# Kernel optimization log

Hardware: AMD Instinct MI355X
Metric: run time of the kernel (lower is better)

Reference implementation:

```python
import jax, jax.numpy as jnp
import numpy as np

B = 2
C = 256
NH = 8
DH = C // NH
NL = 4
NP = 4
NLAYERS = 6
DFF = 1024
SHAPES = [(128, 128), (64, 64), (32, 32), (16, 16)]
LQ = sum(h * w for h, w in SHAPES)
STARTS = np.cumsum([0] + [h * w for h, w in SHAPES])[:-1].tolist()


def _ln(x, g, b, eps=1e-5):
    mu = jnp.mean(x, -1, keepdims=True)
    var = jnp.mean((x - mu) ** 2, -1, keepdims=True)
    return (x - mu) * jax.lax.rsqrt(var + eps) * g + b


def _ref_points():
    # centers of each cell, normalized to [0,1]; valid_ratios == 1 (masks=None path)
    pts = []
    for (h, w) in SHAPES:
        ry = (np.arange(h) + 0.5) / h
        rx = (np.arange(w) + 0.5) / w
        gy, gx = np.meshgrid(ry, rx, indexing='ij')
        pts.append(np.stack([gx.reshape(-1), gy.reshape(-1)], -1))
    return jnp.asarray(np.concatenate(pts, 0), jnp.float32)  # [LQ,2] (x,y)


def _bilinear(vf, loc, Hl, Wl):
    # vf: [B,NH,S,DH] flattened level features; loc: [B,LQ,NH,NP,2] in [0,1]
    # grid_sample semantics: bilinear, zero padding, align_corners=False
    x = loc[..., 0] * Wl - 0.5
    y = loc[..., 1] * Hl - 0.5
    x0 = jnp.floor(x)
    y0 = jnp.floor(y)
    wx = x - x0
    wy = y - y0
    out = 0.0
    for dx, dy, w in ((0, 0, (1 - wx) * (1 - wy)), (1, 0, wx * (1 - wy)),
                      (0, 1, (1 - wx) * wy), (1, 1, wx * wy)):
        xi = x0 + dx
        yi = y0 + dy
        valid = (xi >= 0) & (xi < Wl) & (yi >= 0) & (yi < Hl)
        idx = (jnp.clip(yi, 0, Hl - 1) * Wl + jnp.clip(xi, 0, Wl - 1)).astype(jnp.int32)
        idx = jnp.transpose(idx, (0, 2, 1, 3)).reshape(B, NH, -1)  # [B,NH,LQ*NP]
        g = jnp.take_along_axis(vf, idx[..., None], axis=2)        # [B,NH,LQ*NP,DH]
        wgt = jnp.transpose(w * valid, (0, 2, 1, 3)).reshape(B, NH, -1)
        out = out + g * wgt[..., None]
    return out.reshape(B, NH, LQ, NP, DH)


def _forward(src0, src1, src2, src3, pos0, pos1, pos2, pos3, level_embed,
             Woff, boff, Wattn, battn, Wval, bval, Wout, bout,
             g1, b1, Wff1, bff1, Wff2, bff2, g2, b2):
    srcs = [src0, src1, src2, src3]
    poss = [pos0, pos1, pos2, pos3]
    src = jnp.concatenate([s.reshape(B, C, -1).transpose(0, 2, 1) for s in srcs], 1)
    pos = jnp.concatenate([p.reshape(B, C, -1).transpose(0, 2, 1) + level_embed[l][None, None]
                           for l, p in enumerate(poss)], 1)
    ref = _ref_points()  # [LQ,2]
    norm_wh = jnp.asarray([[w, h] for (h, w) in SHAPES], jnp.float32)  # offset_normalizer
    x = src
    for l in range(NLAYERS):
        q = x + pos
        off = (q @ Woff[l] + boff[l]).reshape(B, LQ, NH, NL, NP, 2)
        attn = jax.nn.softmax((q @ Wattn[l] + battn[l]).reshape(B, LQ, NH, NL * NP), -1)
        attn = attn.reshape(B, LQ, NH, NL, NP)
        val = (x @ Wval[l] + bval[l]).reshape(B, LQ, NH, DH)
        loc = ref[None, :, None, None, None, :] + off / norm_wh[None, None, None, :, None, :]
        out = jnp.zeros((B, NH, LQ, DH), x.dtype)
        for lv, (h, w) in enumerate(SHAPES):
            s0 = STARTS[lv]
            vf = val[:, s0:s0 + h * w].transpose(0, 2, 1, 3)   # [B,NH,S,DH]
            samp = _bilinear(vf, loc[:, :, :, lv], h, w)       # [B,NH,LQ,NP,DH]
            a = attn[:, :, :, lv].transpose(0, 2, 1, 3)        # [B,NH,LQ,NP]
            out = out + jnp.einsum('bhqpd,bhqp->bhqd', samp, a)
        out = out.transpose(0, 2, 1, 3).reshape(B, LQ, C) @ Wout[l] + bout[l]
        x = _ln(x + out, g1[l], b1[l])
        ff = jax.nn.relu(x @ Wff1[l] + bff1[l]) @ Wff2[l] + bff2[l]
        x = _ln(x + ff, g2[l], b2[l])
    return x


def setup_inputs() -> dict:
    key = jax.random.key(0)
    ks = jax.random.split(key, 20)
    d = {}
    for i, (h, w) in enumerate(SHAPES):
        d[f'src{i}'] = jax.random.normal(ks[i], (B, C, h, w), jnp.float32)
        d[f'pos{i}'] = jax.random.normal(ks[4 + i], (B, C, h, w), jnp.float32) * 0.1
    d['level_embed'] = jax.random.normal(ks[8], (NL, C), jnp.float32)

    def lin(k, fi, fo, scale=None):
        s = scale if scale is not None else 1.0 / np.sqrt(fi)
        return jax.random.normal(k, (NLAYERS, fi, fo), jnp.float32) * s

    d['Woff'] = lin(ks[9], C, NH * NL * NP * 2, 0.01)
    d['boff'] = jax.random.uniform(ks[10], (NLAYERS, NH * NL * NP * 2), jnp.float32, -0.5, 0.5)
    d['Wattn'] = lin(ks[11], C, NH * NL * NP)
    d['battn'] = jnp.zeros((NLAYERS, NH * NL * NP), jnp.float32)
    d['Wval'] = lin(ks[12], C, C)
    d['bval'] = jnp.zeros((NLAYERS, C), jnp.float32)
    d['Wout'] = lin(ks[13], C, C)
    d['bout'] = jnp.zeros((NLAYERS, C), jnp.float32)
    d['g1'] = jnp.ones((NLAYERS, C), jnp.float32)
    d['b1'] = jnp.zeros((NLAYERS, C), jnp.float32)
    d['Wff1'] = lin(ks[14], C, DFF)
    d['bff1'] = jnp.zeros((NLAYERS, DFF), jnp.float32)
    d['Wff2'] = lin(ks[15], DFF, C)
    d['bff2'] = jnp.zeros((NLAYERS, C), jnp.float32)
    d['g2'] = jnp.ones((NLAYERS, C), jnp.float32)
    d['b2'] = jnp.zeros((NLAYERS, C), jnp.float32)
    return d


def reference(src0, src1, src2, src3, pos0, pos1, pos2, pos3, level_embed,
              Woff, boff, Wattn, battn, Wval, bval, Wout, bout,
              g1, b1, Wff1, bff1, Wff2, bff2, g2, b2):
    return _forward(src0, src1, src2, src3, pos0, pos1, pos2, pos3, level_embed,
                    Woff, boff, Wattn, battn, Wval, bval, Wout, bout,
                    g1, b1, Wff1, bff1, Wff2, bff2, g2, b2)
```

## Files before the change

kernel.cpp:

```cpp
#include <hip/hip_runtime.h>
#include <hip/hip_bf16.h>
#include <hip/hip_fp16.h>
#include <math.h>

namespace {
constexpr int B_   = 2;
constexpr int C_   = 256;
constexpr int NH_  = 8;
constexpr int DH_  = 32;
constexpr int NP_  = 4;
constexpr int DFF_ = 1024;
constexpr int LQ_  = 21760;
constexpr int M_   = B_ * LQ_;
}

typedef __bf16  bf16x8 __attribute__((ext_vector_type(8)));
typedef short   s16x8  __attribute__((ext_vector_type(8)));
typedef float   f32x4  __attribute__((ext_vector_type(4)));

static __device__ __forceinline__ unsigned short f2bf(float f) {
    return __builtin_bit_cast(unsigned short, __float2bfloat16(f));
}
static __device__ __forceinline__ float bf2f(unsigned short u) {
    return __bfloat162float(__builtin_bit_cast(__hip_bfloat16, u));
}

__global__ void k_wt(const float* __restrict__ in, __hip_bfloat16* __restrict__ out,
                     int K, int N, int outStride)
{
    __shared__ float tile[32][33];
    int n0 = blockIdx.x * 32, k0 = blockIdx.y * 32;
    const float* inl = in + (size_t)blockIdx.z * K * N;
    __hip_bfloat16* outl = out + (size_t)blockIdx.z * outStride;
    for (int i = threadIdx.y; i < 32; i += 8)
        tile[i][threadIdx.x] = inl[(size_t)(k0 + i) * N + n0 + threadIdx.x];
    __syncthreads();
    for (int i = threadIdx.y; i < 32; i += 8)
        outl[(size_t)(n0 + i) * K + k0 + threadIdx.x] = __float2bfloat16(tile[threadIdx.x][i]);
}

__global__ __launch_bounds__(256) void k_assemble2(
    const float* __restrict__ s0, const float* __restrict__ s1,
    const float* __restrict__ s2, const float* __restrict__ s3,
    const float* __restrict__ p0, const float* __restrict__ p1,
    const float* __restrict__ p2, const float* __restrict__ p3,
    const float* __restrict__ lev, float* __restrict__ x,
    __hip_bfloat16* __restrict__ xbf, __hip_bfloat16* __restrict__ posbf,
    __hip_bfloat16* __restrict__ qbf)
{
    int bid = blockIdx.x;
    int lv, rem, HW, S0;
    const float *sp, *pp;
    if (bid < 8192)       { lv = 0; rem = bid;         HW = 16384; S0 = 0;     sp = s0; pp = p0; }
    else if (bid < 10240) { lv = 1; rem = bid - 8192;  HW = 4096;  S0 = 16384; sp = s1; pp = p1; }
    else if (bid < 10752) { lv = 2; rem = bid - 10240; HW = 1024;  S0 = 20480; sp = s2; pp = p2; }
    else                  { lv = 3; rem = bid - 10752; HW = 256;   S0 = 21504; sp = s3; pp = p3; }
    int sptiles = HW >> 5;
    int spt = rem % sptiles;
    int ct  = (rem / sptiles) & 7;
    int b   = rem / (sptiles * 8);
    int sp0 = spt * 32, c0 = ct * 32;

    __shared__ float ts[32][33], tp[32][33];
    int tx = threadIdx.x & 31, ty = threadIdx.x >> 5;
#pragma unroll
    for (int i = 0; i < 4; i++) {
        int c = c0 + ty + i * 8;
        size_t si = ((size_t)(b * C_ + c)) * HW + sp0 + tx;
        ts[ty + i * 8][tx] = sp[si];
        tp[ty + i * 8][tx] = pp[si];
    }
    __syncthreads();
#pragma unroll
    for (int i = 0; i < 4; i++) {
        int s = S0 + sp0 + ty + i * 8;
        int c = c0 + tx;
        float sv = ts[tx][ty + i * 8];
        float pv = tp[tx][ty + i * 8] + lev[lv * C_ + c];
        size_t idx = ((size_t)(b * LQ_ + s)) * C_ + c;
        x[idx]     = sv;
        xbf[idx]   = __float2bfloat16(sv);
        posbf[idx] = __float2bfloat16(pv);
        qbf[idx]   = __float2bfloat16(sv + pv);
    }
}

template<bool RELU, bool BF16OUT>
__global__ __launch_bounds__(256) void k_gemm_mfma(
    const __hip_bfloat16* __restrict__ A,
    const __hip_bfloat16* __restrict__ Wt,
    const float* __restrict__ bias,
    void* __restrict__ Co,
    int M, int N, int K)
{
    __shared__ char As[128 * 128];
    __shared__ char Bs[128 * 128];
    int t = threadIdx.x, w = t >> 6, lane = t & 63;
    int m0 = blockIdx.x * 128, n0 = blockIdx.y * 128;
    int wm = w >> 1, wn = w & 1;

    f32x4 acc[4][4] = {};

    int rowoff  = lane >> 3;
    int colswz  = ((lane & 7) ^ (lane >> 3)) << 3;

    for (int kt = 0; kt < K; kt += 64) {
#pragma unroll
        for (int j = 0; j < 4; j++) {
            int rowbase = w * 32 + j * 8;
            const __hip_bfloat16* srcA = A  + (size_t)(m0 + rowbase + rowoff) * K + kt + colswz;
            const __hip_bfloat16* srcB = Wt + (size_t)(n0 + rowbase + rowoff) * K + kt + colswz;
            __builtin_amdgcn_global_load_lds(
                (const __attribute__((address_space(1))) void*)srcA,
                (__attribute__((address_space(3))) void*)(As + rowbase * 128), 16, 0, 0);
            __builtin_amdgcn_global_load_lds(
                (const __attribute__((address_space(1))) void*)srcB,
                (__attribute__((address_space(3))) void*)(Bs + rowbase * 128), 16, 0, 0);
        }
        __syncthreads();
#pragma unroll
        for (int k0 = 0; k0 < 64; k0 += 32) {
            int kb = k0 * 2 + (lane >> 4) * 16;
            bf16x8 af[4], bfr[4];
#pragma unroll
            for (int mi = 0; mi < 4; mi++) {
                int r = wm * 64 + mi * 16 + (lane & 15);
                s16x8 raw = *(const s16x8*)(As + r * 128 + (kb ^ ((r & 7) << 4)));
                af[mi] = __builtin_bit_cast(bf16x8, raw);
            }
#pragma unroll
            for (int ni = 0; ni < 4; ni++) {
                int r = wn * 64 + ni * 16 + (lane & 15);
                s16x8 raw = *(const s16x8*)(Bs + r * 128 + (kb ^ ((r & 7) << 4)));
                bfr[ni] = __builtin_bit_cast(bf16x8, raw);
            }
#pragma unroll
            for (int mi = 0; mi < 4; mi++)
#pragma unroll
                for (int ni = 0; ni < 4; ni++)
                    acc[mi][ni] = __builtin_amdgcn_mfma_f32_16x16x32_bf16(
                        af[mi], bfr[ni], acc[mi][ni], 0, 0, 0);
        }
        __syncthreads();
    }

#pragma unroll
    for (int ni = 0; ni < 4; ni++) {
        int col = n0 + wn * 64 + ni * 16 + (lane & 15);
        float bb = bias[col];
#pragma unroll
        for (int mi = 0; mi < 4; mi++) {
            int row = m0 + wm * 64 + mi * 16 + ((lane >> 4) << 2);
#pragma unroll
            for (int r = 0; r < 4; r++) {
                float v = acc[mi][ni][r] + bb;
                if (RELU) v = fmaxf(v, 0.f);
                if (BF16OUT)
                    ((__hip_bfloat16*)Co)[(size_t)(row + r) * N + col] = __float2bfloat16(v);
                else
                    ((float*)Co)[(size_t)(row + r) * N + col] = v;
            }
        }
    }
}

__global__ __launch_bounds__(256) void k_gemm_qa(
    const __hip_bfloat16* __restrict__ A,
    const __hip_bfloat16* __restrict__ Wq,
    const float* __restrict__ boff, const float* __restrict__ battn,
    __half* __restrict__ offh, float* __restrict__ attb, int M)
{
    constexpr int K = 256;
    __shared__ char As[128 * 128];
    __shared__ char Bs[128 * 128];
    int t = threadIdx.x, w = t >> 6, lane = t & 63;
    int m0 = blockIdx.x * 128, n0 = blockIdx.y * 128;
    int wm = w >> 1, wn = w & 1;

    f32x4 acc[4][4] = {};
    int rowoff  = lane >> 3;
    int colswz  = ((lane & 7) ^ (lane >> 3)) << 3;

    for (int kt = 0; kt < K; kt += 64) {
#pragma unroll
        for (int j = 0; j < 4; j++) {
            int rowbase = w * 32 + j * 8;
            const __hip_bfloat16* srcA = A  + (size_t)(m0 + rowbase + rowoff) * K + kt + colswz;
            const __hip_bfloat16* srcB = Wq + (size_t)(n0 + rowbase + rowoff) * K + kt + colswz;
            __builtin_amdgcn_global_load_lds(
                (const __attribute__((address_space(1))) void*)srcA,
                (__attribute__((address_space(3))) void*)(As + rowbase * 128), 16, 0, 0);
            __builtin_amdgcn_global_load_lds(
                (const __attribute__((address_space(1))) void*)srcB,
                (__attribute__((address_space(3))) void*)(Bs + rowbase * 128), 16, 0, 0);
        }
        __syncthreads();
#pragma unroll
        for (int k0 = 0; k0 < 64; k0 += 32) {
            int kb = k0 * 2 + (lane >> 4) * 16;
            bf16x8 af[4], bfr[4];
#pragma unroll
            for (int mi = 0; mi < 4; mi++) {
                int r = wm * 64 + mi * 16 + (lane & 15);
                s16x8 raw = *(const s16x8*)(As + r * 128 + (kb ^ ((r & 7) << 4)));
                af[mi] = __builtin_bit_cast(bf16x8, raw);
            }
#pragma unroll
            for (int ni = 0; ni < 4; ni++) {
                int r = wn * 64 + ni * 16 + (lane & 15);
                s16x8 raw = *(const s16x8*)(Bs + r * 128 + (kb ^ ((r & 7) << 4)));
                bfr[ni] = __builtin_bit_cast(bf16x8, raw);
            }
#pragma unroll
            for (int mi = 0; mi < 4; mi++)
#pragma unroll
                for (int ni = 0; ni < 4; ni++)
                    acc[mi][ni] = __builtin_amdgcn_mfma_f32_16x16x32_bf16(
                        af[mi], bfr[ni], acc[mi][ni], 0, 0, 0);
        }
        __syncthreads();
    }

    if (blockIdx.y == 2) {
#pragma unroll
        for (int ni = 0; ni < 4; ni++) {
            int col = wn * 64 + ni * 16 + (lane & 15);
            float bb = battn[col];
#pragma unroll
            for (int mi = 0; mi < 4; mi++) {
                int row = m0 + wm * 64 + mi * 16 + ((lane >> 4) << 2);
#pragma unroll
                for (int r = 0; r < 4; r++)
                    attb[(size_t)(row + r) * 128 + col] = acc[mi][ni][r] + bb;
            }
        }
    } else {
#pragma unroll
        for (int ni = 0; ni < 4; ni++) {
            int col = n0 + wn * 64 + ni * 16 + (lane & 15);
            float bb = boff[col];
#pragma unroll
            for (int mi = 0; mi < 4; mi++) {
                int row = m0 + wm * 64 + mi * 16 + ((lane >> 4) << 2);
#pragma unroll
                for (int r = 0; r < 4; r++)
                    offh[(size_t)(row + r) * 256 + col] = __float2half(acc[mi][ni][r] + bb);
            }
        }
    }
}

template<bool WRITE_Q>
__global__ __launch_bounds__(512) void k_gemm_ln(
    const __hip_bfloat16* __restrict__ A,
    const __hip_bfloat16* __restrict__ Wt,
    const float* __restrict__ bias,
    float* __restrict__ xio,
    __hip_bfloat16* __restrict__ xbf,
    const float* __restrict__ g, const float* __restrict__ beta,
    const __hip_bfloat16* __restrict__ posb,
    __hip_bfloat16* __restrict__ qout,
    int M, int K)
{
    __shared__ char As[2][128 * 128];
    __shared__ char Bs[2][256 * 128];
    __shared__ float sred1[128][4];
    __shared__ float sred2[128][4];

    int t = threadIdx.x, w = t >> 6, lane = t & 63;
    int m0 = blockIdx.x * 128;
    int wm = w >> 2, wn = w & 3;

    f32x4 acc[4][4] = {};

    int rowoff  = lane >> 3;
    int colswz  = ((lane & 7) ^ rowoff) << 3;

    auto STAGE = [&](char* Ab, char* Bb, int kt) {
#pragma unroll
        for (int j = 0; j < 2; j++) {
            int rowbase = w * 16 + j * 8;
            const __hip_bfloat16* srcA = A + (size_t)(m0 + rowbase + rowoff) * K + kt + colswz;
            __builtin_amdgcn_global_load_lds(
                (const __attribute__((address_space(1))) void*)srcA,
                (__attribute__((address_space(3))) void*)(Ab + rowbase * 128), 16, 0, 0);
        }
#pragma unroll
        for (int j = 0; j < 4; j++) {
            int rowbase = w * 32 + j * 8;
            const __hip_bfloat16* srcB = Wt + (size_t)(rowbase + rowoff) * K + kt + colswz;
            __builtin_amdgcn_global_load_lds(
                (const __attribute__((address_space(1))) void*)srcB,
                (__attribute__((address_space(3))) void*)(Bb + rowbase * 128), 16, 0, 0);
        }
    };

    STAGE(As[0], Bs[0], 0);
    asm volatile("s_waitcnt vmcnt(0)" ::: "memory");
    __builtin_amdgcn_s_barrier();

    const int nt = K >> 6;
    int cur = 0;
    for (int tt = 0; tt < nt; ++tt) {
        if (tt + 1 < nt) STAGE(As[cur ^ 1], Bs[cur ^ 1], (tt + 1) << 6);
        const char* Ab = As[cur];
        const char* Bb = Bs[cur];
#pragma unroll
        for (int k0 = 0; k0 < 64; k0 += 32) {
            int kb = k0 * 2 + (lane >> 4) * 16;
            bf16x8 af[4], bfr[4];
#pragma unroll
            for (int mi = 0; mi < 4; mi++) {
                int r = wm * 64 + mi * 16 + (lane & 15);
                s16x8 raw = *(const s16x8*)(Ab + r * 128 + (kb ^ ((r & 7) << 4)));
                af[mi] = __builtin_bit_cast(bf16x8, raw);
            }
#pragma unroll
            for (int ni = 0; ni < 4; ni++) {
                int r = wn * 64 + ni * 16 + (lane & 15);
                s16x8 raw = *(const s16x8*)(Bb + r * 128 + (kb ^ ((r & 7) << 4)));
                bfr[ni] = __builtin_bit_cast(bf16x8, raw);
            }
#pragma unroll
            for (int mi = 0; mi < 4; mi++)
#pragma unroll
                for (int ni = 0; ni < 4; ni++)
                    acc[mi][ni] = __builtin_amdgcn_mfma_f32_16x16x32_bf16(
                        af[mi], bfr[ni], acc[mi][ni], 0, 0, 0);
        }
        asm volatile("s_waitcnt vmcnt(0)" ::: "memory");
        __builtin_amdgcn_s_barrier();
        cur ^= 1;
    }

    int cl = lane & 15;
    int rg = (lane >> 4) << 2;
    float bcol[4], gcol[4], btcol[4];
#pragma unroll
    for (int ni = 0; ni < 4; ni++) {
        int col = wn * 64 + ni * 16 + cl;
        bcol[ni]  = bias[col];
        gcol[ni]  = g[col];
        btcol[ni] = beta[col];
    }

#pragma unroll
    for (int mi = 0; mi < 4; mi++)
#pragma unroll
    for (int r = 0; r < 4; r++) {
        int lr  = wm * 64 + mi * 16 + rg + r;
        int row = m0 + lr;
        float s = 0.f;
#pragma unroll
        for (int ni = 0; ni < 4; ni++) {
            int col = wn * 64 + ni * 16 + cl;
            float v = acc[mi][ni][r] + bcol[ni] + xio[(size_t)row * 256 + col];
            acc[mi][ni][r] = v;
            s += v;
        }
        s += __shfl_xor(s, 1); s += __shfl_xor(s, 2);
        s += __shfl_xor(s, 4); s += __shfl_xor(s, 8);
        if (cl == 0) sred1[lr][wn] = s;
    }
    __syncthreads();

    float mu[4][4];
#pragma unroll
    for (int mi = 0; mi < 4; mi++)
#pragma unroll
    for (int r = 0; r < 4; r++) {
        int lr = wm * 64 + mi * 16 + rg + r;
        mu[mi][r] = (sred1[lr][0] + sred1[lr][1] + sred1[lr][2] + sred1[lr][3]) * (1.f / 256.f);
        float s2 = 0.f;
#pragma unroll
        for (int ni = 0; ni < 4; ni++) {
            float d = acc[mi][ni][r] - mu[mi][r];
            s2 += d * d;
        }
        s2 += __shfl_xor(s2, 1); s2 += __shfl_xor(s2, 2);
        s2 += __shfl_xor(s2, 4); s2 += __shfl_xor(s2, 8);
        if (cl == 0) sred2[lr][wn] = s2;
    }
    __syncthreads();

#pragma unroll
    for (int mi = 0; mi < 4; mi++)
#pragma unroll
    for (int r = 0; r < 4; r++) {
        int lr  = wm * 64 + mi * 16 + rg + r;
        int row = m0 + lr;
        float var = (sred2[lr][0] + sred2[lr][1] + sred2[lr][2] + sred2[lr][3]) * (1.f / 256.f);
        float rstd = rsqrtf(var + 1e-5f);
#pragma unroll
        for (int ni = 0; ni < 4; ni++) {
            int col = wn * 64 + ni * 16 + cl;
            size_t idx = (size_t)row * 256 + col;
            float o = (acc[mi][ni][r] - mu[mi][r]) * rstd * gcol[ni] + btcol[ni];
            xio[idx] = o;
            xbf[idx] = __float2bfloat16(o);
            if (WRITE_Q)
                qout[idx] = __float2bfloat16(o + bf2f(__builtin_bit_cast(unsigned short, posb[idx])));
        }
    }
}

__global__ __launch_bounds__(256) void k_sample4(const __hip_bfloat16* __restrict__ val,
                                                 const __half* __restrict__ offh,
                                                 const float* __restrict__ logits,
                                                 __hip_bfloat16* __restrict__ out)
{
    __shared__ int2 sIW[4 * 64 * 17];

    int t  = threadIdx.x;
    int qb = blockIdx.x;

#pragma unroll
    for (int it = 0; it < 4; it++) {
        int item = t + it * 256;
        int qi = item >> 7;
        int pt = item & 127;
        int bs = qb * 8 + qi;
        int b  = bs / LQ_;
        int s  = bs % LQ_;
        int h  = pt >> 4, lv = (pt >> 2) & 3;

        float lg = logits[(size_t)bs * 128 + pt];
        float mx = lg;
#pragma unroll
        for (int m = 1; m < 16; m <<= 1) mx = fmaxf(mx, __shfl_xor(mx, m));
        float ex = __expf(lg - mx);
        float sm = ex;
#pragma unroll
        for (int m = 1; m < 16; m <<= 1) sm += __shfl_xor(sm, m);
        float aw = ex / sm;

        int p0, Wq;
        if (s < 16384)      { p0 = s;         Wq = 128; }
        else if (s < 20480) { p0 = s - 16384; Wq = 64;  }
        else if (s < 21504) { p0 = s - 20480; Wq = 32;  }
        else                { p0 = s - 21504; Wq = 16;  }
        float invWq = 1.f / (float)Wq;
        float refx = ((p0 % Wq) + 0.5f) * invWq;
        float refy = ((p0 / Wq) + 0.5f) * invWq;

        int W  = 128 >> lv;
        int S0 = (65536 - (65536 >> (2 * lv))) / 3;
        float fW = (float)W;

        __half2 o2 = ((const __half2*)(offh + (size_t)bs * 256))[pt];
        float ox = __low2float(o2), oy = __high2float(o2);
        float xx = refx * fW + ox - 0.5f;
        float yy = refy * fW + oy - 0.5f;
        float x0f = floorf(xx), y0f = floorf(yy);
        float wx = xx - x0f, wy = yy - y0f;
        int x0 = (int)x0f, y0 = (int)y0f;
        int x1 = x0 + 1, y1 = y0 + 1;
        bool vx0 = (x0 >= 0) & (x0 < W), vx1 = (x1 >= 0) & (x1 < W);
        bool vy0 = (y0 >= 0) & (y0 < W), vy1 = (y1 >= 0) & (y1 < W);
        int cx0 = min(max(x0, 0), W - 1), cx1 = min(max(x1, 0), W - 1);
        int cy0 = min(max(y0, 0), W - 1), cy1 = min(max(y1, 0), W - 1);

        int rowbase = (b * LQ_ + S0) * C_ + h * DH_;
        int g  = item >> 4;
        int pj = pt & 15;
        int i00 = (rowbase + (cy0 * W + cx0) * C_) * 2;
        int i10 = (rowbase + (cy0 * W + cx1) * C_) * 2;
        int i01 = (rowbase + (cy1 * W + cx0) * C_) * 2;
        int i11 = (rowbase + (cy1 * W + cx1) * C_) * 2;
        float w00 = aw * (1.f - wx) * (1.f - wy) * ((vx0 & vy0) ? 1.f : 0.f);
        float w10 = aw * wx * (1.f - wy) * ((vx1 & vy0) ? 1.f : 0.f);
        float w01 = aw * (1.f - wx) * wy * ((vx0 & vy1) ? 1.f : 0.f);
        float w11 = aw * wx * wy * ((vx1 & vy1) ? 1.f : 0.f);
        sIW[(0 * 64 + g) * 17 + pj] = make_int2(i00, __float_as_int(w00));
        sIW[(1 * 64 + g) * 17 + pj] = make_int2(i10, __float_as_int(w10));
        sIW[(2 * 64 + g) * 17 + pj] = make_int2(i01, __float_as_int(w01));
        sIW[(3 * 64 + g) * 17 + pj] = make_int2(i11, __float_as_int(w11));
    }
    __syncthreads();

    {
        int g  = t >> 2;
        int dq = t & 3;
        int bs = qb * 8 + (g >> 3);
        int h  = g & 7;
        int dbyte = dq * 16;

        const char* vbase = (const char*)val;
        float a0 = 0.f, a1 = 0.f, a2 = 0.f, a3 = 0.f;
        float a4 = 0.f, a5 = 0.f, a6 = 0.f, a7 = 0.f;
#pragma unroll
        for (int j = 0; j < 16; j++) {
#pragma unroll
            for (int k = 0; k < 4; k++) {
                int2 iw = sIW[(k * 64 + g) * 17 + j];
                float w = __int_as_float(iw.y);
                uint4 u = *(const uint4*)(vbase + iw.x + dbyte);
                a0 = fmaf(w, __builtin_bit_cast(float, u.x << 16), a0);
                a1 = fmaf(w, __builtin_bit_cast(float, u.x & 0xffff0000u), a1);
                a2 = fmaf(w, __builtin_bit_cast(float, u.y << 16), a2);
                a3 = fmaf(w, __builtin_bit_cast(float, u.y & 0xffff0000u), a3);
                a4 = fmaf(w, __builtin_bit_cast(float, u.z << 16), a4);
                a5 = fmaf(w, __builtin_bit_cast(float, u.z & 0xffff0000u), a5);
                a6 = fmaf(w, __builtin_bit_cast(float, u.w << 16), a6);
                a7 = fmaf(w, __builtin_bit_cast(float, u.w & 0xffff0000u), a7);
            }
        }
        uint4 o;
        o.x = (unsigned)f2bf(a0) | ((unsigned)f2bf(a1) << 16);
        o.y = (unsigned)f2bf(a2) | ((unsigned)f2bf(a3) << 16);
        o.z = (unsigned)f2bf(a4) | ((unsigned)f2bf(a5) << 16);
        o.w = (unsigned)f2bf(a6) | ((unsigned)f2bf(a7) << 16);
        *(uint4*)((char*)out + (size_t)bs * 512 + h * 64 + dbyte) = o;
    }
}

extern "C" void kernel_launch(void* const* d_in, const int* in_sizes, int n_in,
                              void* d_out, int out_size, void* d_ws, size_t ws_size,
                              hipStream_t stream)
{
    const float* src_[4] = {(const float*)d_in[0], (const float*)d_in[2],
                            (const float*)d_in[4], (const float*)d_in[6]};
    const float* pos_[4] = {(const float*)d_in[1], (const float*)d_in[3],
                            (const float*)d_in[5], (const float*)d_in[7]};
    const float* lev   = (const float*)d_in[8];
    const float* Woff  = (const float*)d_in[9];
    const float* boff  = (const float*)d_in[10];
    const float* Wattn = (const float*)d_in[11];
    const float* battn = (const float*)d_in[12];
    const float* Wval  = (const float*)d_in[13];
    const float* bval  = (const float*)d_in[14];
    const float* Wout  = (const float*)d_in[15];
    const float* bout  = (const float*)d_in[16];
    const float* g1    = (const float*)d_in[17];
    const float* b1    = (const float*)d_in[18];
    const float* Wff1  = (const float*)d_in[19];
    const float* bff1  = (const float*)d_in[20];
    const float* Wff2  = (const float*)d_in[21];
    const float* bff2  = (const float*)d_in[22];
    const float* g2    = (const float*)d_in[23];
    const float* b2    = (const float*)d_in[24];

    float* x = (float*)d_out;
    size_t MC = (size_t)M_ * C_;

    __hip_bfloat16* pos_bf = (__hip_bfloat16*)d_ws;
    __hip_bfloat16* q_bf   = pos_bf + MC;
    __hip_bfloat16* x_bf   = q_bf + MC;
    __half* offh           = (__half*)(x_bf + MC);
    float*  attb           = (float*)(offh + MC);
    __hip_bfloat16* val_bf = (__hip_bfloat16*)(attb + (size_t)M_ * 128);
    __hip_bfloat16* pad_bf = val_bf + MC;
    __hip_bfloat16* ffh_bf = (__hip_bfloat16*)offh;
    __hip_bfloat16* wbf    = pad_bf + MC;

    __hip_bfloat16* wq    = wbf;
    __hip_bfloat16* wvalt = wq    + 6 * 98304;
    __hip_bfloat16* woutt = wvalt + 6 * 65536;
    __hip_bfloat16* wff1t = woutt + 6 * 65536;
    __hip_bfloat16* wff2t = wff1t + 6 * 262144;

    dim3 blk(256);
    dim3 tblk(32, 8);

    k_wt<<<dim3(8, 8, 6),  tblk, 0, stream>>>(Woff,  wq,               256, 256,  98304);
    k_wt<<<dim3(4, 8, 6),  tblk, 0, stream>>>(Wattn, wq + 256 * 256,   256, 128,  98304);
    k_wt<<<dim3(8, 8, 6),  tblk, 0, stream>>>(Wval,  wvalt,            256, 256,  65536);
    k_wt<<<dim3(8, 8, 6),  tblk, 0, stream>>>(Wout,  woutt,            256, 256,  65536);
    k_wt<<<dim3(32, 8, 6), tblk, 0, stream>>>(Wff1,  wff1t,            256, 1024, 262144);
    k_wt<<<dim3(8, 32, 6), tblk, 0, stream>>>(Wff2,  wff2t,            1024, 256, 262144);

    k_assemble2<<<10880, blk, 0, stream>>>(
        src_[0], src_[1], src_[2], src_[3],
        pos_[0], pos_[1], pos_[2], pos_[3], lev, x, x_bf, pos_bf, q_bf);

    for (int l = 0; l < 6; l++) {
        k_gemm_qa<<<dim3(M_ / 128, 3), blk, 0, stream>>>(
            q_bf, wq + (size_t)l * 98304, boff + l * 256, battn + l * 128,
            offh, attb, M_);

        k_gemm_mfma<false, true><<<dim3(M_ / 128, 2), blk, 0, stream>>>(
            x_bf, wvalt + (size_t)l * 65536, bval + l * 256, val_bf, M_, 256, C_);

        k_sample4<<<M_ / 8, blk, 0, stream>>>(val_bf, offh, attb, q_bf);

        k_gemm_ln<false><<<M_ / 128, 512, 0, stream>>>(
            q_bf, woutt + (size_t)l * 65536, bout + l * 256,
            x, x_bf, g1 + l * 256, b1 + l * 256,
            nullptr, nullptr, M_, C_);

        k_gemm_mfma<true, true><<<dim3(M_ / 128, 8), blk, 0, stream>>>(
            x_bf, wff1t + (size_t)l * 262144, bff1 + l * DFF_, ffh_bf, M_, DFF_, C_);

        if (l < 5)
            k_gemm_ln<true><<<M_ / 128, 512, 0, stream>>>(
                ffh_bf, wff2t + (size_t)l * 262144, bff2 + l * C_,
                x, x_bf, g2 + l * 256, b2 + l * 256,
                pos_bf, q_bf, M_, DFF_);
        else
            k_gemm_ln<false><<<M_ / 128, 512, 0, stream>>>(
                ffh_bf, wff2t + (size_t)l * 262144, bff2 + l * C_,
                x, x_bf, g2 + l * 256, b2 + l * 256,
                nullptr, nullptr, M_, DFF_);
    }
}
```

Measured before the change: 1.808 ms.

## Fuse FFN up/down GEMMs into one kernel and shrink output-projection tiles

Replaces the separate FF1 GEMM, FF2 GEMM and LayerNorm launches with one fused k_ff kernel. It keeps each 64-row activation tile in LDS, computes the hidden layer in 128-wide chunks with ReLU into LDS, and accumulates the FF2 output directly, so the 1024-wide hidden tensor never goes through global memory. The output projection also moves to a 64-row k_out kernel that stages the full input tile once. Both kernels read weights straight from global memory without LDS staging, which relies on cache hits, and run fewer waves per block than the previous 512-thread kernel.

```diff
diff --git a/kernel.cpp b/kernel.cpp
--- a/kernel.cpp
+++ b/kernel.cpp
@@ -17,6 +17,9 @@
 typedef __bf16  bf16x8 __attribute__((ext_vector_type(8)));
 typedef short   s16x8  __attribute__((ext_vector_type(8)));
 typedef float   f32x4  __attribute__((ext_vector_type(4)));
+
+#define AS1 __attribute__((address_space(1)))
+#define AS3 __attribute__((address_space(3)))
 
 static __device__ __forceinline__ unsigned short f2bf(float f) {
     return __builtin_bit_cast(unsigned short, __float2bfloat16(f));
@@ -111,11 +114,9 @@
             const __hip_bfloat16* srcA = A  + (size_t)(m0 + rowbase + rowoff) * K + kt + colswz;
             const __hip_bfloat16* srcB = Wt + (size_t)(n0 + rowbase + rowoff) * K + kt + colswz;
             __builtin_amdgcn_global_load_lds(
-                (const __attribute__((address_space(1))) void*)srcA,
-                (__attribute__((address_space(3))) void*)(As + rowbase * 128), 16, 0, 0);
+                (const AS1 void*)srcA, (AS3 void*)(As + rowbase * 128), 16, 0, 0);
             __builtin_amdgcn_global_load_lds(
-                (const __attribute__((address_space(1))) void*)srcB,
-                (__attribute__((address_space(3))) void*)(Bs + rowbase * 128), 16, 0, 0);
+                (const AS1 void*)srcB, (AS3 void*)(Bs + rowbase * 128), 16, 0, 0);
         }
         __syncthreads();
 #pragma unroll
@@ -188,11 +189,9 @@
             const __hip_bfloat16* srcA = A  + (size_t)(m0 + rowbase + rowoff) * K + kt + colswz;
             const __hip_bfloat16* srcB = Wq + (size_t)(n0 + rowbase + rowoff) * K + kt + colswz;
             __builtin_amdgcn_global_load_lds(
-                (const __attribute__((address_space(1))) void*)srcA,
-                (__attribute__((address_space(3))) void*)(As + rowbase * 128), 16, 0, 0);
+                (const AS1 void*)srcA, (AS3 void*)(As + rowbase * 128), 16, 0, 0);
             __builtin_amdgcn_global_load_lds(
-                (const __attribute__((address_space(1))) void*)srcB,
-                (__attribute__((address_space(3))) void*)(Bs + rowbase * 128), 16, 0, 0);
+                (const AS1 void*)srcB, (AS3 void*)(Bs + rowbase * 128), 16, 0, 0);
         }
         __syncthreads();
 #pragma unroll
@@ -251,94 +250,19 @@
 }
 
 template<bool WRITE_Q>
-__global__ __launch_bounds__(512) void k_gemm_ln(
-    const __hip_bfloat16* __restrict__ A,
-    const __hip_bfloat16* __restrict__ Wt,
-    const float* __restrict__ bias,
-    float* __restrict__ xio,
-    __hip_bfloat16* __restrict__ xbf,
-    const float* __restrict__ g, const float* __restrict__ beta,
-    const __hip_bfloat16* __restrict__ posb,
-    __hip_bfloat16* __restrict__ qout,
-    int M, int K)
-{
-    __shared__ char As[2][128 * 128];
-    __shared__ char Bs[2][256 * 128];
-    __shared__ float sred1[128][4];
-    __shared__ float sred2[128][4];
-
-    int t = threadIdx.x, w = t >> 6, lane = t & 63;
-    int m0 = blockIdx.x * 128;
-    int wm = w >> 2, wn = w & 3;
-
-    f32x4 acc[4][4] = {};
-
-    int rowoff  = lane >> 3;
-    int colswz  = ((lane & 7) ^ rowoff) << 3;
-
-    auto STAGE = [&](char* Ab, char* Bb, int kt) {
-#pragma unroll
-        for (int j = 0; j < 2; j++) {
-            int rowbase = w * 16 + j * 8;
-            const __hip_bfloat16* srcA = A + (size_t)(m0 + rowbase + rowoff) * K + kt + colswz;
-            __builtin_amdgcn_global_load_lds(
-                (const __attribute__((address_space(1))) void*)srcA,
-                (__attribute__((address_space(3))) void*)(Ab + rowbase * 128), 16, 0, 0);
-        }
-#pragma unroll
-        for (int j = 0; j < 4; j++) {
-            int rowbase = w * 32 + j * 8;
-            const __hip_bfloat16* srcB = Wt + (size_t)(rowbase + rowoff) * K + kt + colswz;
-            __builtin_amdgcn_global_load_lds(
-                (const __attribute__((address_space(1))) void*)srcB,
-                (__attribute__((address_space(3))) void*)(Bb + rowbase * 128), 16, 0, 0);
-        }
-    };
-
-    STAGE(As[0], Bs[0], 0);
-    asm volatile("s_waitcnt vmcnt(0)" ::: "memory");
-    __builtin_amdgcn_s_barrier();
-
-    const int nt = K >> 6;
-    int cur = 0;
-    for (int tt = 0; tt < nt; ++tt) {
-        if (tt + 1 < nt) STAGE(As[cur ^ 1], Bs[cur ^ 1], (tt + 1) << 6);
-        const char* Ab = As[cur];
-        const char* Bb = Bs[cur];
-#pragma unroll
-        for (int k0 = 0; k0 < 64; k0 += 32) {
-            int kb = k0 * 2 + (lane >> 4) * 16;
-            bf16x8 af[4], bfr[4];
-#pragma unroll
-            for (int mi = 0; mi < 4; mi++) {
-                int r = wm * 64 + mi * 16 + (lane & 15);
-                s16x8 raw = *(const s16x8*)(Ab + r * 128 + (kb ^ ((r & 7) << 4)));
-                af[mi] = __builtin_bit_cast(bf16x8, raw);
-            }
-#pragma unroll
-            for (int ni = 0; ni < 4; ni++) {
-                int r = wn * 64 + ni * 16 + (lane & 15);
-                s16x8 raw = *(const s16x8*)(Bb + r * 128 + (kb ^ ((r & 7) << 4)));
-                bfr[ni] = __builtin_bit_cast(bf16x8, raw);
-            }
-#pragma unroll
-            for (int mi = 0; mi < 4; mi++)
-#pragma unroll
-                for (int ni = 0; ni < 4; ni++)
-                    acc[mi][ni] = __builtin_amdgcn_mfma_f32_16x16x32_bf16(
-                        af[mi], bfr[ni], acc[mi][ni], 0, 0, 0);
-        }
-        asm volatile("s_waitcnt vmcnt(0)" ::: "memory");
-        __builtin_amdgcn_s_barrier();
-        cur ^= 1;
-    }
-
+static __device__ __forceinline__ void ln_epilogue64(
+    f32x4 (&acc)[4][4], int m0, int w, int lane,
+    const float* bias, float* xio, __hip_bfloat16* xbf,
+    const float* g, const float* beta,
+    const __hip_bfloat16* posb, __hip_bfloat16* qout,
+    float (*sred1)[4], float (*sred2)[4])
+{
     int cl = lane & 15;
     int rg = (lane >> 4) << 2;
     float bcol[4], gcol[4], btcol[4];
 #pragma unroll
     for (int ni = 0; ni < 4; ni++) {
-        int col = wn * 64 + ni * 16 + cl;
+        int col = w * 64 + ni * 16 + cl;
         bcol[ni]  = bias[col];
         gcol[ni]  = g[col];
         btcol[ni] = beta[col];
@@ -348,19 +272,19 @@
     for (int mi = 0; mi < 4; mi++)
 #pragma unroll
     for (int r = 0; r < 4; r++) {
-        int lr  = wm * 64 + mi * 16 + rg + r;
+        int lr  = mi * 16 + rg + r;
         int row = m0 + lr;
         float s = 0.f;
 #pragma unroll
         for (int ni = 0; ni < 4; ni++) {
-            int col = wn * 64 + ni * 16 + cl;
+            int col = w * 64 + ni * 16 + cl;
             float v = acc[mi][ni][r] + bcol[ni] + xio[(size_t)row * 256 + col];
             acc[mi][ni][r] = v;
             s += v;
         }
         s += __shfl_xor(s, 1); s += __shfl_xor(s, 2);
         s += __shfl_xor(s, 4); s += __shfl_xor(s, 8);
-        if (cl == 0) sred1[lr][wn] = s;
+        if (cl == 0) sred1[lr][w] = s;
     }
     __syncthreads();
 
@@ -369,7 +293,7 @@
     for (int mi = 0; mi < 4; mi++)
 #pragma unroll
     for (int r = 0; r < 4; r++) {
-        int lr = wm * 64 + mi * 16 + rg + r;
+        int lr = mi * 16 + rg + r;
         mu[mi][r] = (sred1[lr][0] + sred1[lr][1] + sred1[lr][2] + sred1[lr][3]) * (1.f / 256.f);
         float s2 = 0.f;
 #pragma unroll
@@ -379,7 +303,7 @@
         }
         s2 += __shfl_xor(s2, 1); s2 += __shfl_xor(s2, 2);
         s2 += __shfl_xor(s2, 4); s2 += __shfl_xor(s2, 8);
-        if (cl == 0) sred2[lr][wn] = s2;
+        if (cl == 0) sred2[lr][w] = s2;
     }
     __syncthreads();
 
@@ -387,13 +311,13 @@
     for (int mi = 0; mi < 4; mi++)
 #pragma unroll
     for (int r = 0; r < 4; r++) {
-        int lr  = wm * 64 + mi * 16 + rg + r;
+        int lr  = mi * 16 + rg + r;
         int row = m0 + lr;
         float var = (sred2[lr][0] + sred2[lr][1] + sred2[lr][2] + sred2[lr][3]) * (1.f / 256.f);
         float rstd = rsqrtf(var + 1e-5f);
 #pragma unroll
         for (int ni = 0; ni < 4; ni++) {
-            int col = wn * 64 + ni * 16 + cl;
+            int col = w * 64 + ni * 16 + cl;
             size_t idx = (size_t)row * 256 + col;
             float o = (acc[mi][ni][r] - mu[mi][r]) * rstd * gcol[ni] + btcol[ni];
             xio[idx] = o;
@@ -402,6 +326,165 @@
                 qout[idx] = __float2bfloat16(o + bf2f(__builtin_bit_cast(unsigned short, posb[idx])));
         }
     }
+}
+
+static __device__ __forceinline__ void stage_x64(
+    const __hip_bfloat16* __restrict__ src, int m0, char* xs, int w, int lane)
+{
+    int r  = lane >> 5;
+    int gl = lane & 31;
+#pragma unroll
+    for (int j = 0; j < 8; j++) {
+        int row = (j * 4 + w) * 2 + r;
+        int gsw = gl ^ (row & 7);
+        const __hip_bfloat16* s = src + (size_t)(m0 + row) * 256 + gsw * 8;
+        __builtin_amdgcn_global_load_lds(
+            (const AS1 void*)s, (AS3 void*)(xs + (j * 4 + w) * 1024), 16, 0, 0);
+    }
+}
+
+template<bool WRITE_Q>
+__global__ __launch_bounds__(256) void k_out(
+    const __hip_bfloat16* __restrict__ A,
+    const __hip_bfloat16* __restrict__ Wt,
+    const float* __restrict__ bias,
+    float* __restrict__ xio, __hip_bfloat16* __restrict__ xbf,
+    const float* __restrict__ g, const float* __restrict__ beta,
+    const __hip_bfloat16* __restrict__ posb, __hip_bfloat16* __restrict__ qout)
+{
+    __shared__ char xs[64 * 512];
+    __shared__ float sred1[64][4];
+    __shared__ float sred2[64][4];
+
+    int t = threadIdx.x, w = t >> 6, lane = t & 63;
+    int m0 = blockIdx.x * 64;
+
+    stage_x64(A, m0, xs, w, lane);
+    asm volatile("s_waitcnt vmcnt(0)" ::: "memory");
+    __builtin_amdgcn_s_barrier();
+
+    f32x4 acc[4][4] = {};
+#pragma unroll
+    for (int k0 = 0; k0 < 256; k0 += 32) {
+        int kb = k0 * 2 + (lane >> 4) * 16;
+        bf16x8 af[4], bw[4];
+#pragma unroll
+        for (int mi = 0; mi < 4; mi++) {
+            int r = mi * 16 + (lane & 15);
+            s16x8 raw = *(const s16x8*)(xs + r * 512 + (kb ^ ((r & 7) << 4)));
+            af[mi] = __builtin_bit_cast(bf16x8, raw);
+        }
+#pragma unroll
+        for (int ni = 0; ni < 4; ni++) {
+            int out = w * 64 + ni * 16 + (lane & 15);
+            bw[ni] = *(const bf16x8*)(Wt + (size_t)out * 256 + k0 + (lane >> 4) * 8);
+        }
+#pragma unroll
+        for (int mi = 0; mi < 4; mi++)
+#pragma unroll
+            for (int ni = 0; ni < 4; ni++)
+                acc[mi][ni] = __builtin_amdgcn_mfma_f32_16x16x32_bf16(
+                    af[mi], bw[ni], acc[mi][ni], 0, 0, 0);
+    }
+    __syncthreads();
+
+    ln_epilogue64<WRITE_Q>(acc, m0, w, lane, bias, xio, xbf, g, beta, posb, qout,
+                           sred1, sred2);
+}
+
+template<bool WRITE_Q>
+__global__ __launch_bounds__(256, 2) void k_ff(
+    const __hip_bfloat16* __restrict__ xin,
+    const __hip_bfloat16* __restrict__ w1t,
+    const float* __restrict__ b1v,
+    const __hip_bfloat16* __restrict__ w2t,
+    const float* __restrict__ b2v,
+    float* __restrict__ xio, __hip_bfloat16* __restrict__ xbf,
+    const float* __restrict__ g, const float* __restrict__ beta,
+    const __hip_bfloat16* __restrict__ posb, __hip_bfloat16* __restrict__ qout)
+{
+    __shared__ char xs[64 * 512];
+    __shared__ char hs[64 * 256];
+    __shared__ float sred1[64][4];
+    __shared__ float sred2[64][4];
+
+    int t = threadIdx.x, w = t >> 6, lane = t & 63;
+    int m0 = blockIdx.x * 64;
+
+    stage_x64(xin, m0, xs, w, lane);
+    asm volatile("s_waitcnt vmcnt(0)" ::: "memory");
+    __builtin_amdgcn_s_barrier();
+
+    f32x4 acc2[4][4] = {};
+
+    for (int hc = 0; hc < 8; hc++) {
+        f32x4 acc1[4][2] = {};
+#pragma unroll
+        for (int k0 = 0; k0 < 256; k0 += 32) {
+            int kb = k0 * 2 + (lane >> 4) * 16;
+            bf16x8 af[4], b1f[2];
+#pragma unroll
+            for (int mi = 0; mi < 4; mi++) {
+                int r = mi * 16 + (lane & 15);
+                s16x8 raw = *(const s16x8*)(xs + r * 512 + (kb ^ ((r & 7) << 4)));
+                af[mi] = __builtin_bit_cast(bf16x8, raw);
+            }
+#pragma unroll
+            for (int ni = 0; ni < 2; ni++) {
+                int hid = hc * 128 + w * 32 + ni * 16 + (lane & 15);
+                b1f[ni] = *(const bf16x8*)(w1t + (size_t)hid * 256 + k0 + (lane >> 4) * 8);
+            }
+#pragma unroll
+            for (int mi = 0; mi < 4; mi++)
+#pragma unroll
+                for (int ni = 0; ni < 2; ni++)
+                    acc1[mi][ni] = __builtin_amdgcn_mfma_f32_16x16x32_bf16(
+                        af[mi], b1f[ni], acc1[mi][ni], 0, 0, 0);
+        }
+
+#pragma unroll
+        for (int ni = 0; ni < 2; ni++) {
+            int hidl = w * 32 + ni * 16 + (lane & 15);
+            float bb = b1v[hc * 128 + hidl];
+#pragma unroll
+            for (int mi = 0; mi < 4; mi++)
+#pragma unroll
+            for (int r = 0; r < 4; r++) {
+                int row = mi * 16 + ((lane >> 4) << 2) + r;
+                float v = fmaxf(acc1[mi][ni][r] + bb, 0.f);
+                int byte = row * 256 + ((hidl * 2) ^ ((row & 7) << 4));
+                *(unsigned short*)(hs + byte) = f2bf(v);
+            }
+        }
+        __syncthreads();
+
+#pragma unroll
+        for (int k0 = 0; k0 < 128; k0 += 32) {
+            int kb = k0 * 2 + (lane >> 4) * 16;
+            bf16x8 ah[4], bw[4];
+#pragma unroll
+            for (int mi = 0; mi < 4; mi++) {
+                int r = mi * 16 + (lane & 15);
+                s16x8 raw = *(const s16x8*)(hs + r * 256 + (kb ^ ((r & 7) << 4)));
+                ah[mi] = __builtin_bit_cast(bf16x8, raw);
+            }
+#pragma unroll
+            for (int ni = 0; ni < 4; ni++) {
+                int out = w * 64 + ni * 16 + (lane & 15);
+                bw[ni] = *(const bf16x8*)(w2t + (size_t)out * 1024 + hc * 128 + k0 + (lane >> 4) * 8);
+            }
+#pragma unroll
+            for (int mi = 0; mi < 4; mi++)
+#pragma unroll
+                for (int ni = 0; ni < 4; ni++)
+                    acc2[mi][ni] = __builtin_amdgcn_mfma_f32_16x16x32_bf16(
+                        ah[mi], bw[ni], acc2[mi][ni], 0, 0, 0);
+        }
+        __syncthreads();
+    }
+
+    ln_epilogue64<WRITE_Q>(acc2, m0, w, lane, b2v, xio, xbf, g, beta, posb, qout,
+                           sred1, sred2);
 }
 
 __global__ __launch_bounds__(256) void k_sample4(const __hip_bfloat16* __restrict__ val,
@@ -549,9 +632,7 @@
     __half* offh           = (__half*)(x_bf + MC);
     float*  attb           = (float*)(offh + MC);
     __hip_bfloat16* val_bf = (__hip_bfloat16*)(attb + (size_t)M_ * 128);
-    __hip_bfloat16* pad_bf = val_bf + MC;
-    __hip_bfloat16* ffh_bf = (__hip_bfloat16*)offh;
-    __hip_bfloat16* wbf    = pad_bf + MC;
+    __hip_bfloat16* wbf    = val_bf + MC;
 
     __hip_bfloat16* wq    = wbf;
     __hip_bfloat16* wvalt = wq    + 6 * 98304;
@@ -583,23 +664,19 @@
 
         k_sample4<<<M_ / 8, blk, 0, stream>>>(val_bf, offh, attb, q_bf);
 
-        k_gemm_ln<false><<<M_ / 128, 512, 0, stream>>>(
+        k_out<false><<<M_ / 64, blk, 0, stream>>>(
             q_bf, woutt + (size_t)l * 65536, bout + l * 256,
-            x, x_bf, g1 + l * 256, b1 + l * 256,
-            nullptr, nullptr, M_, C_);
-
-        k_gemm_mfma<true, true><<<dim3(M_ / 128, 8), blk, 0, stream>>>(
-            x_bf, wff1t + (size_t)l * 262144, bff1 + l * DFF_, ffh_bf, M_, DFF_, C_);
+            x, x_bf, g1 + l * 256, b1 + l * 256, nullptr, nullptr);
 
         if (l < 5)
-            k_gemm_ln<true><<<M_ / 128, 512, 0, stream>>>(
-                ffh_bf, wff2t + (size_t)l * 262144, bff2 + l * C_,
-                x, x_bf, g2 + l * 256, b2 + l * 256,
-                pos_bf, q_bf, M_, DFF_);
+            k_ff<true><<<M_ / 64, blk, 0, stream>>>(
+                x_bf, wff1t + (size_t)l * 262144, bff1 + l * DFF_,
+                wff2t + (size_t)l * 262144, bff2 + l * C_,
+                x, x_bf, g2 + l * 256, b2 + l * 256, pos_bf, q_bf);
         else
-            k_gemm_ln<false><<<M_ / 128, 512, 0, stream>>>(
-                ffh_bf, wff2t + (size_t)l * 262144, bff2 + l * C_,
-                x, x_bf, g2 + l * 256, b2 + l * 256,
-                nullptr, nullptr, M_, DFF_);
-    }
-}
+            k_ff<false><<<M_ / 64, blk, 0, stream>>>(
+                x_bf, wff1t + (size_t)l * 262144, bff1 + l * DFF_,
+                wff2t + (size_t)l * 262144, bff2 + l * C_,
+                x, x_bf, g2 + l * 256, b2 + l * 256, nullptr, nullptr);
+    }
+}
```

Result: slower. 1.874 ms (+3.6%).

## Load LN-GEMM weights directly from global in MFMA fragment layout, drop LDS B staging

Applied to the files above, without the earlier changes.

Adds a weight pre-transform kernel that writes the Wout and Wff2 weights in a fragment-ordered layout, so each lane reads its 8-element bf16 B operand straight from global memory. The fused GEMM+LayerNorm kernel no longer stages B through LDS. This cuts LDS use from about 96KB to about 32KB per block, which may allow more resident blocks and fewer LDS writes. The cost is that B loads now go through global/L2 on every k-step with no LDS reuse across waves, and the latency of those loads is exposed.

```diff
diff --git a/kernel.cpp b/kernel.cpp
--- a/kernel.cpp
+++ b/kernel.cpp
@@ -18,6 +18,9 @@
 typedef short   s16x8  __attribute__((ext_vector_type(8)));
 typedef float   f32x4  __attribute__((ext_vector_type(4)));
 
+#define AS1 __attribute__((address_space(1)))
+#define AS3 __attribute__((address_space(3)))
+
 static __device__ __forceinline__ unsigned short f2bf(float f) {
     return __builtin_bit_cast(unsigned short, __float2bfloat16(f));
 }
@@ -37,6 +40,29 @@
     __syncthreads();
     for (int i = threadIdx.y; i < 32; i += 8)
         outl[(size_t)(n0 + i) * K + k0 + threadIdx.x] = __float2bfloat16(tile[threadIdx.x][i]);
+}
+
+__global__ void k_wt2(const float* __restrict__ in, __hip_bfloat16* __restrict__ out,
+                      int K, int N, int outStride)
+{
+    __shared__ float tile[32][65];
+    int col0 = blockIdx.x * 64;
+    int k0   = blockIdx.y * 32;
+    const float* inl = in + (size_t)blockIdx.z * K * N;
+    __hip_bfloat16* outl = out + (size_t)blockIdx.z * outStride;
+    int t = threadIdx.x;
+#pragma unroll
+    for (int p = 0; p < 8; p++) {
+        int s = t + p * 256;
+        tile[s >> 6][s & 63] = inl[(size_t)(k0 + (s >> 6)) * N + col0 + (s & 63)];
+    }
+    __syncthreads();
+    size_t base = ((size_t)(k0 >> 5) * N + col0) * 32;
+#pragma unroll
+    for (int p = 0; p < 8; p++) {
+        int s = t + p * 256;
+        outl[base + s] = __float2bfloat16(tile[s & 31][(s >> 5) & 63]);
+    }
 }
 
 __global__ __launch_bounds__(256) void k_assemble2(
@@ -111,11 +137,9 @@
             const __hip_bfloat16* srcA = A  + (size_t)(m0 + rowbase + rowoff) * K + kt + colswz;
             const __hip_bfloat16* srcB = Wt + (size_t)(n0 + rowbase + rowoff) * K + kt + colswz;
             __builtin_amdgcn_global_load_lds(
-                (const __attribute__((address_space(1))) void*)srcA,
-                (__attribute__((address_space(3))) void*)(As + rowbase * 128), 16, 0, 0);
+                (const AS1 void*)srcA, (AS3 void*)(As + rowbase * 128), 16, 0, 0);
             __builtin_amdgcn_global_load_lds(
-                (const __attribute__((address_space(1))) void*)srcB,
-                (__attribute__((address_space(3))) void*)(Bs + rowbase * 128), 16, 0, 0);
+                (const AS1 void*)srcB, (AS3 void*)(Bs + rowbase * 128), 16, 0, 0);
         }
         __syncthreads();
 #pragma unroll
@@ -188,11 +212,9 @@
             const __hip_bfloat16* srcA = A  + (size_t)(m0 + rowbase + rowoff) * K + kt + colswz;
             const __hip_bfloat16* srcB = Wq + (size_t)(n0 + rowbase + rowoff) * K + kt + colswz;
             __builtin_amdgcn_global_load_lds(
-                (const __attribute__((address_space(1))) void*)srcA,
-                (__attribute__((address_space(3))) void*)(As + rowbase * 128), 16, 0, 0);
+                (const AS1 void*)srcA, (AS3 void*)(As + rowbase * 128), 16, 0, 0);
             __builtin_amdgcn_global_load_lds(
-                (const __attribute__((address_space(1))) void*)srcB,
-                (__attribute__((address_space(3))) void*)(Bs + rowbase * 128), 16, 0, 0);
+                (const AS1 void*)srcB, (AS3 void*)(Bs + rowbase * 128), 16, 0, 0);
         }
         __syncthreads();
 #pragma unroll
@@ -251,19 +273,16 @@
 }
 
 template<bool WRITE_Q>
-__global__ __launch_bounds__(512) void k_gemm_ln(
+__global__ __launch_bounds__(512) void k_gemm_lnf(
     const __hip_bfloat16* __restrict__ A,
-    const __hip_bfloat16* __restrict__ Wt,
+    const __hip_bfloat16* __restrict__ Wf,
     const float* __restrict__ bias,
-    float* __restrict__ xio,
-    __hip_bfloat16* __restrict__ xbf,
+    float* __restrict__ xio, __hip_bfloat16* __restrict__ xbf,
     const float* __restrict__ g, const float* __restrict__ beta,
-    const __hip_bfloat16* __restrict__ posb,
-    __hip_bfloat16* __restrict__ qout,
+    const __hip_bfloat16* __restrict__ posb, __hip_bfloat16* __restrict__ qout,
     int M, int K)
 {
     __shared__ char As[2][128 * 128];
-    __shared__ char Bs[2][256 * 128];
     __shared__ float sred1[128][4];
     __shared__ float sred2[128][4];
 
@@ -272,43 +291,34 @@
     int wm = w >> 2, wn = w & 3;
 
     f32x4 acc[4][4] = {};
-
-    int rowoff  = lane >> 3;
-    int colswz  = ((lane & 7) ^ rowoff) << 3;
-
-    auto STAGE = [&](char* Ab, char* Bb, int kt) {
+    int rowoff = lane >> 3;
+    int colswz = ((lane & 7) ^ rowoff) << 3;
+    int gq = lane >> 4;
+
+    auto STAGE_A = [&](char* Ab, int kt) {
 #pragma unroll
         for (int j = 0; j < 2; j++) {
             int rowbase = w * 16 + j * 8;
             const __hip_bfloat16* srcA = A + (size_t)(m0 + rowbase + rowoff) * K + kt + colswz;
             __builtin_amdgcn_global_load_lds(
-                (const __attribute__((address_space(1))) void*)srcA,
-                (__attribute__((address_space(3))) void*)(Ab + rowbase * 128), 16, 0, 0);
-        }
-#pragma unroll
-        for (int j = 0; j < 4; j++) {
-            int rowbase = w * 32 + j * 8;
-            const __hip_bfloat16* srcB = Wt + (size_t)(rowbase + rowoff) * K + kt + colswz;
-            __builtin_amdgcn_global_load_lds(
-                (const __attribute__((address_space(1))) void*)srcB,
-                (__attribute__((address_space(3))) void*)(Bb + rowbase * 128), 16, 0, 0);
+                (const AS1 void*)srcA, (AS3 void*)(Ab + rowbase * 128), 16, 0, 0);
         }
     };
 
-    STAGE(As[0], Bs[0], 0);
+    STAGE_A(As[0], 0);
     asm volatile("s_waitcnt vmcnt(0)" ::: "memory");
     __builtin_amdgcn_s_barrier();
 
     const int nt = K >> 6;
     int cur = 0;
     for (int tt = 0; tt < nt; ++tt) {
-        if (tt + 1 < nt) STAGE(As[cur ^ 1], Bs[cur ^ 1], (tt + 1) << 6);
+        if (tt + 1 < nt) STAGE_A(As[cur ^ 1], (tt + 1) << 6);
         const char* Ab = As[cur];
-        const char* Bb = Bs[cur];
 #pragma unroll
         for (int k0 = 0; k0 < 64; k0 += 32) {
-            int kb = k0 * 2 + (lane >> 4) * 16;
-            bf16x8 af[4], bfr[4];
+            int ks = tt * 2 + (k0 >> 5);
+            int kb = k0 * 2 + gq * 16;
+            bf16x8 af[4], bw[4];
 #pragma unroll
             for (int mi = 0; mi < 4; mi++) {
                 int r = wm * 64 + mi * 16 + (lane & 15);
@@ -317,16 +327,15 @@
             }
 #pragma unroll
             for (int ni = 0; ni < 4; ni++) {
-                int r = wn * 64 + ni * 16 + (lane & 15);
-                s16x8 raw = *(const s16x8*)(Bb + r * 128 + (kb ^ ((r & 7) << 4)));
-                bfr[ni] = __builtin_bit_cast(bf16x8, raw);
+                int col = wn * 64 + ni * 16 + (lane & 15);
+                bw[ni] = *(const bf16x8*)(Wf + (((size_t)ks * 256 + col) << 5) + (gq << 3));
             }
 #pragma unroll
             for (int mi = 0; mi < 4; mi++)
 #pragma unroll
                 for (int ni = 0; ni < 4; ni++)
                     acc[mi][ni] = __builtin_amdgcn_mfma_f32_16x16x32_bf16(
-                        af[mi], bfr[ni], acc[mi][ni], 0, 0, 0);
+                        af[mi], bw[ni], acc[mi][ni], 0, 0, 0);
         }
         asm volatile("s_waitcnt vmcnt(0)" ::: "memory");
         __builtin_amdgcn_s_barrier();
@@ -555,19 +564,19 @@
 
     __hip_bfloat16* wq    = wbf;
     __hip_bfloat16* wvalt = wq    + 6 * 98304;
-    __hip_bfloat16* woutt = wvalt + 6 * 65536;
-    __hip_bfloat16* wff1t = woutt + 6 * 65536;
-    __hip_bfloat16* wff2t = wff1t + 6 * 262144;
+    __hip_bfloat16* woutf = wvalt + 6 * 65536;
+    __hip_bfloat16* wff1t = woutf + 6 * 65536;
+    __hip_bfloat16* wff2f = wff1t + 6 * 262144;
 
     dim3 blk(256);
     dim3 tblk(32, 8);
 
-    k_wt<<<dim3(8, 8, 6),  tblk, 0, stream>>>(Woff,  wq,               256, 256,  98304);
-    k_wt<<<dim3(4, 8, 6),  tblk, 0, stream>>>(Wattn, wq + 256 * 256,   256, 128,  98304);
-    k_wt<<<dim3(8, 8, 6),  tblk, 0, stream>>>(Wval,  wvalt,            256, 256,  65536);
-    k_wt<<<dim3(8, 8, 6),  tblk, 0, stream>>>(Wout,  woutt,            256, 256,  65536);
-    k_wt<<<dim3(32, 8, 6), tblk, 0, stream>>>(Wff1,  wff1t,            256, 1024, 262144);
-    k_wt<<<dim3(8, 32, 6), tblk, 0, stream>>>(Wff2,  wff2t,            1024, 256, 262144);
+    k_wt<<<dim3(8, 8, 6),  tblk, 0, stream>>>(Woff,  wq,             256, 256,  98304);
+    k_wt<<<dim3(4, 8, 6),  tblk, 0, stream>>>(Wattn, wq + 256 * 256, 256, 128,  98304);
+    k_wt<<<dim3(8, 8, 6),  tblk, 0, stream>>>(Wval,  wvalt,          256, 256,  65536);
+    k_wt<<<dim3(32, 8, 6), tblk, 0, stream>>>(Wff1,  wff1t,          256, 1024, 262144);
+    k_wt2<<<dim3(4, 8, 6),  blk, 0, stream>>>(Wout,  woutf,          256, 256,  65536);
+    k_wt2<<<dim3(4, 32, 6), blk, 0, stream>>>(Wff2,  wff2f,          1024, 256, 262144);
 
     k_assemble2<<<10880, blk, 0, stream>>>(
         src_[0], src_[1], src_[2], src_[3],
@@ -583,23 +592,20 @@
 
         k_sample4<<<M_ / 8, blk, 0, stream>>>(val_bf, offh, attb, q_bf);
 
-        k_gemm_ln<false><<<M_ / 128, 512, 0, stream>>>(
-            q_bf, woutt + (size_t)l * 65536, bout + l * 256,
-            x, x_bf, g1 + l * 256, b1 + l * 256,
-            nullptr, nullptr, M_, C_);
+        k_gemm_lnf<false><<<M_ / 128, 512, 0, stream>>>(
+            q_bf, woutf + (size_t)l * 65536, bout + l * 256,
+            x, x_bf, g1 + l * 256, b1 + l * 256, nullptr, nullptr, M_, 256);
 
         k_gemm_mfma<true, true><<<dim3(M_ / 128, 8), blk, 0, stream>>>(
             x_bf, wff1t + (size_t)l * 262144, bff1 + l * DFF_, ffh_bf, M_, DFF_, C_);
 
         if (l < 5)
-            k_gemm_ln<true><<<M_ / 128, 512, 0, stream>>>(
-                ffh_bf, wff2t + (size_t)l * 262144, bff2 + l * C_,
-                x, x_bf, g2 + l * 256, b2 + l * 256,
-                pos_bf, q_bf, M_, DFF_);
+            k_gemm_lnf<true><<<M_ / 128, 512, 0, stream>>>(
+                ffh_bf, wff2f + (size_t)l * 262144, bff2 + l * C_,
+                x, x_bf, g2 + l * 256, b2 + l * 256, pos_bf, q_bf, M_, DFF_);
         else
-            k_gemm_ln<false><<<M_ / 128, 512, 0, stream>>>(
-                ffh_bf, wff2t + (size_t)l * 262144, bff2 + l * C_,
-                x, x_bf, g2 + l * 256, b2 + l * 256,
-                nullptr, nullptr, M_, DFF_);
-    }
-}
+            k_gemm_lnf<false><<<M_ / 128, 512, 0, stream>>>(
+                ffh_bf, wff2f + (size_t)l * 262144, bff2 + l * C_,
+                x, x_bf, g2 + l * 256, b2 + l * 256, nullptr, nullptr, M_, DFF_);
+    }
+}
```

Measured after the change: 1.876 ms. 1.04x slower.
